# Kernel tuning notes

Measured on AMD Instinct MI355X. Metric: run time of the kernel, lower is better.

The kernel has to match this reference:

```python
import jax, jax.numpy as jnp
import numpy as np
import math

D_MODEL = 2048
N_HEADS = 16
D_K = D_MODEL // N_HEADS


def setup_inputs() -> dict:
    key = jax.random.key(0)
    ks = jax.random.split(key, 10)
    B, S = 1, 2048
    scale = 1.0 / math.sqrt(D_MODEL)
    x = jax.random.normal(ks[0], (B, S, D_MODEL), dtype=jnp.float32)
    mask = jnp.ones((1, 1, S, S), dtype=bool)
    Wq = jax.random.normal(ks[1], (D_MODEL, D_MODEL), dtype=jnp.float32) * scale
    bq = jnp.zeros((D_MODEL,), dtype=jnp.float32)
    Wk = jax.random.normal(ks[2], (D_MODEL, D_MODEL), dtype=jnp.float32) * scale
    bk = jnp.zeros((D_MODEL,), dtype=jnp.float32)
    Wv = jax.random.normal(ks[3], (D_MODEL, D_MODEL), dtype=jnp.float32) * scale
    bv = jnp.zeros((D_MODEL,), dtype=jnp.float32)
    Wo = jax.random.normal(ks[4], (D_MODEL, D_MODEL), dtype=jnp.float32) * scale
    bo = jnp.zeros((D_MODEL,), dtype=jnp.float32)
    return {"x": x, "mask": mask, "Wq": Wq, "bq": bq, "Wk": Wk, "bk": bk,
            "Wv": Wv, "bv": bv, "Wo": Wo, "bo": bo}


def reference(x, mask, Wq, bq, Wk, bk, Wv, bv, Wo, bo):
    B, S, D = x.shape
    # projections (nn.Linear: y = x @ W.T + b; here W stored as [in, out] so x @ W + b)
    def proj(W, b):
        y = x @ W + b                                   # [B, S, D]
        return y.reshape(B, S, N_HEADS, D_K).transpose(0, 2, 1, 3)  # [B, H, S, d_k]
    Q = proj(Wq, bq)
    K = proj(Wk, bk)
    V = proj(Wv, bv)
    scores = jnp.einsum('bhqd,bhkd->bhqk', Q, K) / math.sqrt(D_K)  # [B, H, S, S]
    scores = jnp.where(mask, scores, -jnp.inf)
    attn = jax.nn.softmax(scores, axis=-1)
    out = jnp.einsum('bhqk,bhkd->bhqd', attn, V)        # [B, H, S, d_k]
    out = out.transpose(0, 2, 1, 3).reshape(B, S, D)    # [B, S, D]
    return out @ Wo + bo
```

## Files before the change

kernel.cpp:

```cpp
#include <hip/hip_runtime.h>
#include <cstdint>
#include <cstddef>

typedef __bf16 bf16;
typedef bf16 bf16x8 __attribute__((ext_vector_type(8)));
typedef bf16 bf16x4 __attribute__((ext_vector_type(4)));
typedef bf16 bf16x2 __attribute__((ext_vector_type(2)));
typedef float f32x4 __attribute__((ext_vector_type(4)));
typedef float f32x16 __attribute__((ext_vector_type(16)));
typedef uint32_t u32x4 __attribute__((ext_vector_type(4)));

#define AS1 __attribute__((address_space(1)))
#define AS3 __attribute__((address_space(3)))

constexpr int DMODEL = 2048;
constexpr int SEQ    = 2048;
constexpr int DK     = 128;
constexpr float QSCALE_LOG2E = 0.12751740f;

__global__ __launch_bounds__(256) void cvt_x_kernel(const float* __restrict__ x,
                                                    bf16* __restrict__ xb) {
  size_t i = (size_t)blockIdx.x * 256 + threadIdx.x;
  const float4 a = ((const float4*)x)[i * 2];
  const float4 b = ((const float4*)x)[i * 2 + 1];
  bf16x8 v;
  v[0] = (bf16)a.x; v[1] = (bf16)a.y; v[2] = (bf16)a.z; v[3] = (bf16)a.w;
  v[4] = (bf16)b.x; v[5] = (bf16)b.y; v[6] = (bf16)b.z; v[7] = (bf16)b.w;
  *(bf16x8*)(xb + i * 8) = v;
}

__global__ __launch_bounds__(256) void transpose_w_kernel(
    const float* __restrict__ W0, const float* __restrict__ W1,
    const float* __restrict__ W2, const float* __restrict__ W3,
    bf16* __restrict__ T0, bf16* __restrict__ T1,
    bf16* __restrict__ T2, bf16* __restrict__ T3) {
  int z = blockIdx.x >> 10;
  int t = blockIdx.x & 1023;
  int bi = t >> 5, bj = t & 31;
  const float* W = (z == 0) ? W0 : (z == 1) ? W1 : (z == 2) ? W2 : W3;
  bf16* T        = (z == 0) ? T0 : (z == 1) ? T1 : (z == 2) ? T2 : T3;

  __shared__ float tile[64][68];
  int tid = threadIdx.x;
  int tr = tid >> 4, tc = tid & 15;
#pragma unroll
  for (int i = 0; i < 4; i++) {
    float4 v = *(const float4*)(W + (size_t)(bi * 64 + tr + i * 16) * DMODEL + bj * 64 + tc * 4);
    *(float4*)&tile[tr + i * 16][tc * 4] = v;
  }
  __syncthreads();
  int nl = tid >> 2, kc = (tid & 3) * 16;
  bf16x8 o0, o1;
#pragma unroll
  for (int j = 0; j < 8; j++) {
    o0[j] = (bf16)tile[kc + j][nl];
    o1[j] = (bf16)tile[kc + 8 + j][nl];
  }
  bf16* dst = T + (size_t)(bj * 64 + nl) * DMODEL + bi * 64 + kc;
  *(bf16x8*)dst       = o0;
  *(bf16x8*)(dst + 8) = o1;
}

template <int KIND>
__global__ __launch_bounds__(256) void gemm_bt_kernel(
    const bf16* __restrict__ A,
    const bf16* __restrict__ Bt0, const float* __restrict__ bias0, bf16* __restrict__ outB0,
    const bf16* __restrict__ Bt1, const float* __restrict__ bias1, bf16* __restrict__ outB1,
    const bf16* __restrict__ Bt2, const float* __restrict__ bias2, bf16* __restrict__ outB2,
    float* __restrict__ outF) {
  __shared__ bf16 Als[128 * 64];
  __shared__ bf16 Bls[128 * 64];

  int zt, t;
  if constexpr (KIND == 0) { zt = blockIdx.x >> 8; t = blockIdx.x & 255; }
  else                     { zt = 0;               t = blockIdx.x;       }

  const bf16* Btp; const float* bias;
  if constexpr (KIND == 0) {
    Btp  = (zt == 0) ? Bt0 : (zt == 1) ? Bt1 : Bt2;
    bias = (zt == 0) ? bias0 : (zt == 1) ? bias1 : bias2;
  } else { Btp = Bt0; bias = bias0; }

  int tm = t >> 4, tn = t & 15;
  int m0 = tm * 128, n0 = tn * 128;
  int tid = threadIdx.x;
  int w = tid >> 6, l = tid & 63;
  int wm = w >> 1, wn = w & 1;
  int g = l >> 4, r16 = l & 15;

  f32x4 acc[4][4];
#pragma unroll
  for (int i = 0; i < 4; i++)
#pragma unroll
    for (int j = 0; j < 4; j++) acc[i][j] = (f32x4){0.f, 0.f, 0.f, 0.f};

  int lrow = l >> 3;
  for (int kt = 0; kt < DMODEL / 64; kt++) {
    const bf16* abase = A   + (size_t)m0 * DMODEL + kt * 64;
    const bf16* bbase = Btp + (size_t)n0 * DMODEL + kt * 64;
#pragma unroll
    for (int i = 0; i < 4; i++) {
      int chunk = w * 4 + i;
      int row   = chunk * 8 + lrow;
      int slot  = (l & 7) ^ (row & 7);
      __builtin_amdgcn_global_load_lds((const AS1 void*)(abase + (size_t)row * DMODEL + slot * 8),
                                       (AS3 void*)(Als + chunk * 512), 16, 0, 0);
      __builtin_amdgcn_global_load_lds((const AS1 void*)(bbase + (size_t)row * DMODEL + slot * 8),
                                       (AS3 void*)(Bls + chunk * 512), 16, 0, 0);
    }
    __syncthreads();
#pragma unroll
    for (int ks = 0; ks < 2; ks++) {
      bf16x8 af[4], bfr[4];
#pragma unroll
      for (int mf = 0; mf < 4; mf++) {
        int row  = wm * 64 + mf * 16 + r16;
        int slot = (ks * 4 + g) ^ (row & 7);
        af[mf] = *(const bf16x8*)(Als + row * 64 + slot * 8);
      }
#pragma unroll
      for (int nf = 0; nf < 4; nf++) {
        int row  = wn * 64 + nf * 16 + r16;
        int slot = (ks * 4 + g) ^ (row & 7);
        bfr[nf] = *(const bf16x8*)(Bls + row * 64 + slot * 8);
      }
#pragma unroll
      for (int mf = 0; mf < 4; mf++)
#pragma unroll
        for (int nf = 0; nf < 4; nf++)
          acc[mf][nf] = __builtin_amdgcn_mfma_f32_16x16x32_bf16(af[mf], bfr[nf], acc[mf][nf], 0, 0, 0);
    }
    __syncthreads();
  }

  float bval[4];
#pragma unroll
  for (int nf = 0; nf < 4; nf++) bval[nf] = bias[n0 + wn * 64 + nf * 16 + r16];

  if constexpr (KIND == 1) {
#pragma unroll
    for (int mf = 0; mf < 4; mf++)
#pragma unroll
      for (int nf = 0; nf < 4; nf++)
#pragma unroll
        for (int r = 0; r < 4; r++)
          outF[(size_t)(m0 + wm * 64 + mf * 16 + g * 4 + r) * DMODEL + n0 + wn * 64 + nf * 16 + r16] =
              acc[mf][nf][r] + bval[nf];
  } else {
    if (zt == 2) {
#pragma unroll
      for (int mf = 0; mf < 4; mf++)
#pragma unroll
        for (int nf = 0; nf < 4; nf++) {
          bf16x4 pk;
#pragma unroll
          for (int r = 0; r < 4; r++) pk[r] = (bf16)(acc[mf][nf][r] + bval[nf]);
          *(bf16x4*)(outB2 + (size_t)(n0 + wn * 64 + nf * 16 + r16) * SEQ + m0 + wm * 64 + mf * 16 + g * 4) = pk;
        }
    } else {
      bf16* outp = (zt == 0) ? outB0 : outB1;
      float scl  = (zt == 0) ? QSCALE_LOG2E : 1.0f;
#pragma unroll
      for (int mf = 0; mf < 4; mf++)
#pragma unroll
        for (int nf = 0; nf < 4; nf++)
#pragma unroll
          for (int r = 0; r < 4; r++)
            outp[(size_t)(m0 + wm * 64 + mf * 16 + g * 4 + r) * DMODEL + n0 + wn * 64 + nf * 16 + r16] =
                (bf16)((acc[mf][nf][r] + bval[nf]) * scl);
    }
  }
}

__global__ __launch_bounds__(256, 2) void attn_kernel(const bf16* __restrict__ Q,
                                                      const bf16* __restrict__ K,
                                                      const bf16* __restrict__ Vt,
                                                      float* __restrict__ Opart,
                                                      float* __restrict__ Mp,
                                                      float* __restrict__ Lp) {
  constexpr int NT = 1024 / 64;
  int bx = blockIdx.x;
  int qt = bx >> 5;
  int hh = bx & 31;
  int h = hh >> 1, half = hh & 1;
  int tid = threadIdx.x;
  int w = tid >> 6, l = tid & 63;
  int q5 = l & 31, h5 = l >> 5;

  __shared__ bf16 KL[2][8192];
  __shared__ bf16 VL[2][8192];

  int q0 = qt * 128 + w * 32;

  const bf16* ksrc[4];
  const bf16* vsrc[4];
#pragma unroll
  for (int i = 0; i < 4; i++) {
    int unit = i * 256 + tid;
    ksrc[i] = K  + (size_t)(half * 1024 + (unit & 63)) * DMODEL + h * DK + (unit >> 6) * 8;
    vsrc[i] = Vt + (size_t)(h * DK + (unit & 127)) * SEQ + half * 1024 + (unit >> 7) * 8;
  }

#define ATTN_STAGE(BUF)                                                        \
  {                                                                            \
    _Pragma("unroll")                                                          \
    for (int i_ = 0; i_ < 4; i_++) {                                           \
      __builtin_amdgcn_global_load_lds((const AS1 void*)ksrc[i_],              \
          (AS3 void*)(&KL[BUF][(i_ * 256 + tid) * 8]), 16, 0, 0);              \
      ksrc[i_] += 64 * DMODEL;                                                 \
      __builtin_amdgcn_global_load_lds((const AS1 void*)vsrc[i_],              \
          (AS3 void*)(&VL[BUF][(i_ * 256 + tid) * 8]), 16, 0, 0);              \
      vsrc[i_] += 64;                                                          \
    }                                                                          \
  }

  bf16x8 qb[8];
  {
    const bf16* qbase = Q + (size_t)(q0 + q5) * DMODEL + h * DK + h5 * 8;
#pragma unroll
    for (int kc = 0; kc < 8; kc++) qb[kc] = *(const bf16x8*)(qbase + kc * 16);
  }

  f32x16 o[4];
#pragma unroll
  for (int vf = 0; vf < 4; vf++)
#pragma unroll
    for (int i = 0; i < 16; i++) o[vf][i] = 0.f;
  float mrow = -1e30f, lrow = 0.f;

  ATTN_STAGE(0);
  __syncthreads();

  for (int kb = 0; kb < NT; kb++) {
    int cur = kb & 1;
    if (kb + 1 < NT) ATTN_STAGE(cur ^ 1);

    const bf16* KB = &KL[cur][0];
    f32x16 s0, s1;
#pragma unroll
    for (int i = 0; i < 16; i++) { s0[i] = 0.f; s1[i] = 0.f; }
#pragma unroll
    for (int kc = 0; kc < 8; kc++) {
      bf16x8 k0 = *(const bf16x8*)(KB + ((kc * 2 + h5) * 64 + q5) * 8);
      bf16x8 k1 = *(const bf16x8*)(KB + ((kc * 2 + h5) * 64 + 32 + q5) * 8);
      s0 = __builtin_amdgcn_mfma_f32_32x32x16_bf16(k0, qb[kc], s0, 0, 0, 0);
      s1 = __builtin_amdgcn_mfma_f32_32x32x16_bf16(k1, qb[kc], s1, 0, 0, 0);
    }

    float tm8[8];
#pragma unroll
    for (int i = 0; i < 8; i++)
      tm8[i] = fmaxf(fmaxf(s0[i], s0[i + 8]), fmaxf(s1[i], s1[i + 8]));
#pragma unroll
    for (int i = 0; i < 4; i++) tm8[i] = fmaxf(tm8[i], tm8[i + 4]);
    float bm = fmaxf(fmaxf(tm8[0], tm8[2]), fmaxf(tm8[1], tm8[3]));
    bm = fmaxf(bm, __shfl_xor(bm, 32));

    if (!__all(bm <= mrow + 11.0f)) {
      float mn = fmaxf(mrow, bm);
      float al = exp2f(mrow - mn);
      mrow = mn;
      lrow *= al;
#pragma unroll
      for (int vf = 0; vf < 4; vf++)
#pragma unroll
        for (int i = 0; i < 16; i++) o[vf][i] *= al;
    }

#pragma unroll
    for (int i = 0; i < 16; i++) s0[i] = exp2f(s0[i] - mrow);
#pragma unroll
    for (int i = 0; i < 16; i++) s1[i] = exp2f(s1[i] - mrow);
    float ta[8];
#pragma unroll
    for (int i = 0; i < 8; i++) ta[i] = (s0[i] + s0[i + 8]) + (s1[i] + s1[i + 8]);
#pragma unroll
    for (int i = 0; i < 4; i++) ta[i] += ta[i + 4];
    float ps = (ta[0] + ta[2]) + (ta[1] + ta[3]);
    ps += __shfl_xor(ps, 32);
    lrow += ps;

    uint32_t u[16];
#pragma unroll
    for (int rp = 0; rp < 8; rp++) {
      bf16x2 t0; t0[0] = (bf16)s0[2 * rp]; t0[1] = (bf16)s0[2 * rp + 1];
      u[rp] = __builtin_bit_cast(uint32_t, t0);
      bf16x2 t1; t1[0] = (bf16)s1[2 * rp]; t1[1] = (bf16)s1[2 * rp + 1];
      u[8 + rp] = __builtin_bit_cast(uint32_t, t1);
    }
#pragma unroll
    for (int b = 0; b < 16; b += 4) {
      asm volatile("v_permlane32_swap_b32 %0, %1" : "+v"(u[b]),     "+v"(u[b + 2]));
      asm volatile("v_permlane32_swap_b32 %0, %1" : "+v"(u[b + 1]), "+v"(u[b + 3]));
    }

    const bf16* VB = &VL[cur][0];
#pragma unroll
    for (int ks = 0; ks < 4; ks++) {
      u32x4 tw = {u[ks * 4], u[ks * 4 + 1], u[ks * 4 + 2], u[ks * 4 + 3]};
      bf16x8 pb = __builtin_bit_cast(bf16x8, tw);
#pragma unroll
      for (int vf = 0; vf < 4; vf++) {
        bf16x8 vv = *(const bf16x8*)(VB + ((ks * 2 + h5) * 128 + vf * 32 + q5) * 8);
        o[vf] = __builtin_amdgcn_mfma_f32_32x32x16_bf16(vv, pb, o[vf], 0, 0, 0);
      }
    }
    __syncthreads();
  }

  float* obase = Opart + ((size_t)hh * SEQ + q0 + q5) * DK + h5 * 4;
#pragma unroll
  for (int vf = 0; vf < 4; vf++)
#pragma unroll
    for (int rr = 0; rr < 4; rr++) {
      float4 pk;
      pk.x = o[vf][rr * 4 + 0]; pk.y = o[vf][rr * 4 + 1];
      pk.z = o[vf][rr * 4 + 2]; pk.w = o[vf][rr * 4 + 3];
      *(float4*)(obase + vf * 32 + rr * 8) = pk;
    }
  if (h5 == 0) {
    Mp[(size_t)hh * SEQ + q0 + q5] = mrow;
    Lp[(size_t)hh * SEQ + q0 + q5] = lrow;
  }
#undef ATTN_STAGE
}

__global__ __launch_bounds__(256) void attn_merge_kernel(const float* __restrict__ Opart,
                                                         const float* __restrict__ Mp,
                                                         const float* __restrict__ Lp,
                                                         bf16* __restrict__ AO) {
  size_t idx = (size_t)blockIdx.x * 256 + threadIdx.x;
  int d8 = idx & 15;
  int q  = (int)((idx >> 4) & 2047);
  int h  = (int)(idx >> 15);
  size_t ra = (size_t)(h * 2) * SEQ + q;
  size_t rb = (size_t)(h * 2 + 1) * SEQ + q;
  float ma = Mp[ra], mb = Mp[rb];
  float la = Lp[ra], lb = Lp[rb];
  float m  = fmaxf(ma, mb);
  float wa = exp2f(ma - m), wb = exp2f(mb - m);
  float inv = 1.0f / (la * wa + lb * wb);
  wa *= inv; wb *= inv;
  const float4* A = (const float4*)(Opart + ra * DK + d8 * 8);
  const float4* B = (const float4*)(Opart + rb * DK + d8 * 8);
  float4 a0 = A[0], a1 = A[1], b0 = B[0], b1 = B[1];
  bf16x8 r;
  r[0] = (bf16)(a0.x * wa + b0.x * wb);
  r[1] = (bf16)(a0.y * wa + b0.y * wb);
  r[2] = (bf16)(a0.z * wa + b0.z * wb);
  r[3] = (bf16)(a0.w * wa + b0.w * wb);
  r[4] = (bf16)(a1.x * wa + b1.x * wb);
  r[5] = (bf16)(a1.y * wa + b1.y * wb);
  r[6] = (bf16)(a1.z * wa + b1.z * wb);
  r[7] = (bf16)(a1.w * wa + b1.w * wb);
  *(bf16x8*)(AO + (size_t)q * DMODEL + h * DK + d8 * 8) = r;
}

extern "C" void kernel_launch(void* const* d_in, const int* in_sizes, int n_in,
                              void* d_out, int out_size, void* d_ws, size_t ws_size,
                              hipStream_t stream) {
  const float* x  = (const float*)d_in[0];
  const float* Wq = (const float*)d_in[2];
  const float* bq = (const float*)d_in[3];
  const float* Wk = (const float*)d_in[4];
  const float* bk = (const float*)d_in[5];
  const float* Wv = (const float*)d_in[6];
  const float* bv = (const float*)d_in[7];
  const float* Wo = (const float*)d_in[8];
  const float* bo = (const float*)d_in[9];
  float* out = (float*)d_out;

  const size_t MAT = (size_t)DMODEL * DMODEL;
  bf16* p   = (bf16*)d_ws;
  bf16* xb  = p; p += MAT;
  bf16* Wqt = p; p += MAT;
  bf16* Wkt = p; p += MAT;
  bf16* Wvt = p; p += MAT;
  bf16* Wot = p; p += MAT;
  bf16* Qb  = p; p += MAT;
  bf16* Kb  = p; p += MAT;
  bf16* Vtb = p; p += MAT;
  bf16* AOb = p; p += MAT;
  float* Opart = (float*)xb;
  float* Mpart = (float*)p; p += 512 * 1024 / 2;
  float* Lpart = (float*)p;

  cvt_x_kernel<<<2048, 256, 0, stream>>>(x, xb);
  transpose_w_kernel<<<4096, 256, 0, stream>>>(Wq, Wk, Wv, Wo, Wqt, Wkt, Wvt, Wot);
  gemm_bt_kernel<0><<<768, 256, 0, stream>>>(xb, Wqt, bq, Qb, Wkt, bk, Kb, Wvt, bv, Vtb, nullptr);
  attn_kernel<<<512, 256, 0, stream>>>(Qb, Kb, Vtb, Opart, Mpart, Lpart);
  attn_merge_kernel<<<2048, 256, 0, stream>>>(Opart, Mpart, Lpart, AOb);
  gemm_bt_kernel<1><<<256, 256, 0, stream>>>(AOb, Wot, bo, nullptr,
                                             nullptr, nullptr, nullptr,
                                             nullptr, nullptr, nullptr, out);
}
```

Measured before the change: 207.7 us.

## Replace QKV projection GEMM with 256x256-tile pipelined LDS-direct kernel

Adds a new fused QKV projection kernel that uses 256x256 output tiles with 512 threads. It double-buffers LDS filled by direct global-to-LDS loads with XOR swizzling, interleaves staging with MFMA quadrants, and raises MFMA wave priority with s_setprio. The goal is more operand reuse per tile and better overlap of memory traffic with matrix math. The cost is that only 192 blocks launch, which may underfill the GPU's compute units, and the large LDS and register footprint may limit occupancy.

Result: faster. 197.8 us (-4.8%).

```diff
diff --git a/kernel.cpp b/kernel.cpp
--- a/kernel.cpp
+++ b/kernel.cpp
@@ -59,6 +59,162 @@
   bf16* dst = T + (size_t)(bj * 64 + nl) * DMODEL + bi * 64 + kc;
   *(bf16x8*)dst       = o0;
   *(bf16x8*)(dst + 8) = o1;
+}
+
+__global__ __launch_bounds__(512, 2) void gemm256_qkv_kernel(
+    const bf16* __restrict__ A,
+    const bf16* __restrict__ Bt0, const float* __restrict__ bias0, bf16* __restrict__ outQ,
+    const bf16* __restrict__ Bt1, const float* __restrict__ bias1, bf16* __restrict__ outK,
+    const bf16* __restrict__ Bt2, const float* __restrict__ bias2, bf16* __restrict__ outV) {
+  constexpr int NT = DMODEL / 64;
+  __shared__ bf16 Asl[2][16384];
+  __shared__ bf16 Bsl[2][16384];
+
+  int zt = blockIdx.x >> 6;
+  int t  = blockIdx.x & 63;
+  int tm = t >> 3, tn = t & 7;
+  int m0 = tm * 256, n0 = tn * 256;
+  const bf16* Btp   = (zt == 0) ? Bt0 : (zt == 1) ? Bt1 : Bt2;
+  const float* bias = (zt == 0) ? bias0 : (zt == 1) ? bias1 : bias2;
+
+  int tid = threadIdx.x;
+  int w = tid >> 6, l = tid & 63;
+  int wm = w >> 2, wn = w & 3;
+  int g = l >> 4, r16 = l & 15;
+
+  int u0 = tid, u1 = 512 + tid;
+  int r0 = u0 >> 3, s0 = u0 & 7;
+  int r1 = u1 >> 3, s1 = u1 & 7;
+  const bf16* aS0 = A + (size_t)(m0 + r0) * DMODEL + (s0 ^ (r0 & 7)) * 8;
+  const bf16* aS1 = A + (size_t)(m0 + r1) * DMODEL + (s1 ^ (r1 & 7)) * 8;
+  const bf16* bS0 = Btp + (size_t)(n0 + r0) * DMODEL + (s0 ^ (r0 & 7)) * 8;
+  const bf16* bS1 = Btp + (size_t)(n0 + r1) * DMODEL + (s1 ^ (r1 & 7)) * 8;
+
+  auto STAGE = [&](int tile, int h) {
+    if (tile >= NT) return;
+    int buf = tile & 1;
+    size_t roff = (size_t)(h & 1) * 128 * DMODEL + (size_t)tile * 64;
+    if (h < 2) {
+      __builtin_amdgcn_global_load_lds((const AS1 void*)(aS0 + roff),
+          (AS3 void*)(&Asl[buf][(h & 1) * 8192 + u0 * 8]), 16, 0, 0);
+      __builtin_amdgcn_global_load_lds((const AS1 void*)(aS1 + roff),
+          (AS3 void*)(&Asl[buf][(h & 1) * 8192 + u1 * 8]), 16, 0, 0);
+    } else {
+      __builtin_amdgcn_global_load_lds((const AS1 void*)(bS0 + roff),
+          (AS3 void*)(&Bsl[buf][(h & 1) * 8192 + u0 * 8]), 16, 0, 0);
+      __builtin_amdgcn_global_load_lds((const AS1 void*)(bS1 + roff),
+          (AS3 void*)(&Bsl[buf][(h & 1) * 8192 + u1 * 8]), 16, 0, 0);
+    }
+  };
+
+  bf16x8 afq[2][8];
+  bf16x8 bfn[2][4];
+  f32x4 acc[8][4];
+#pragma unroll
+  for (int i = 0; i < 8; i++)
+#pragma unroll
+    for (int j = 0; j < 4; j++) acc[i][j] = (f32x4){0.f, 0.f, 0.f, 0.f};
+
+#define G256_LDA(MQ, BUF)                                                      \
+  _Pragma("unroll")                                                            \
+  for (int mf = 0; mf < 4; mf++) {                                             \
+    int row = wm * 128 + (MQ) * 64 + mf * 16 + r16;                            \
+    _Pragma("unroll")                                                          \
+    for (int ks = 0; ks < 2; ks++)                                             \
+      afq[MQ][mf * 2 + ks] =                                                   \
+          *(const bf16x8*)(&Asl[BUF][row * 64 + (((ks * 4 + g) ^ (row & 7)) * 8)]); \
+  }
+#define G256_LDB(NQ, BUF)                                                      \
+  _Pragma("unroll")                                                            \
+  for (int nf = 0; nf < 2; nf++) {                                             \
+    int row = wn * 64 + (NQ) * 32 + nf * 16 + r16;                             \
+    _Pragma("unroll")                                                          \
+    for (int ks = 0; ks < 2; ks++)                                             \
+      bfn[NQ][nf * 2 + ks] =                                                   \
+          *(const bf16x8*)(&Bsl[BUF][row * 64 + (((ks * 4 + g) ^ (row & 7)) * 8)]); \
+  }
+#define G256_MMA(MQ, NQ)                                                       \
+  _Pragma("unroll")                                                            \
+  for (int mf = 0; mf < 4; mf++)                                               \
+    _Pragma("unroll")                                                          \
+    for (int nf = 0; nf < 2; nf++)                                             \
+      _Pragma("unroll")                                                        \
+      for (int ks = 0; ks < 2; ks++)                                           \
+        acc[(MQ) * 4 + mf][(NQ) * 2 + nf] =                                    \
+            __builtin_amdgcn_mfma_f32_16x16x32_bf16(afq[MQ][mf * 2 + ks],      \
+                bfn[NQ][nf * 2 + ks], acc[(MQ) * 4 + mf][(NQ) * 2 + nf], 0, 0, 0);
+#define G256_BAR() __builtin_amdgcn_s_barrier()
+#define G256_P1()  __builtin_amdgcn_s_setprio(1)
+#define G256_P0()  __builtin_amdgcn_s_setprio(0)
+
+  STAGE(0, 0); STAGE(0, 1); STAGE(0, 2); STAGE(0, 3);
+  STAGE(1, 0); STAGE(1, 1);
+  asm volatile("s_waitcnt vmcnt(4)" ::: "memory");
+  G256_BAR();
+
+  for (int it = 0; it < NT / 2; ++it) {
+    int t1 = 2 * it + 1, t2 = 2 * it + 2, t3 = 2 * it + 3;
+    G256_LDA(0, 0) G256_LDB(0, 0)
+    STAGE(t1, 2);
+    G256_BAR(); G256_P1(); G256_MMA(0, 0) G256_P0(); G256_BAR();
+    G256_LDA(1, 0) G256_LDB(1, 0)
+    STAGE(t1, 3);
+    G256_BAR(); G256_P1(); G256_MMA(1, 0) G256_P0(); G256_BAR();
+    STAGE(t2, 0);
+    G256_BAR(); G256_P1(); G256_MMA(0, 1) G256_P0(); G256_BAR();
+    STAGE(t2, 1);
+    G256_BAR(); G256_P1(); G256_MMA(1, 1) G256_P0();
+    if (it < NT / 2 - 1) asm volatile("s_waitcnt vmcnt(4)" ::: "memory");
+    else                 asm volatile("s_waitcnt vmcnt(0)" ::: "memory");
+    G256_BAR();
+    G256_LDA(0, 1) G256_LDB(0, 1)
+    STAGE(t2, 2);
+    G256_BAR(); G256_P1(); G256_MMA(0, 0) G256_P0(); G256_BAR();
+    G256_LDA(1, 1) G256_LDB(1, 1)
+    STAGE(t2, 3);
+    G256_BAR(); G256_P1(); G256_MMA(1, 0) G256_P0(); G256_BAR();
+    STAGE(t3, 0);
+    G256_BAR(); G256_P1(); G256_MMA(0, 1) G256_P0(); G256_BAR();
+    STAGE(t3, 1);
+    G256_BAR(); G256_P1(); G256_MMA(1, 1) G256_P0();
+    if (it < NT / 2 - 1) asm volatile("s_waitcnt vmcnt(4)" ::: "memory");
+    G256_BAR();
+  }
+
+  float bval[4];
+#pragma unroll
+  for (int nf = 0; nf < 4; nf++) bval[nf] = bias[n0 + wn * 64 + nf * 16 + r16];
+
+  if (zt == 2) {
+#pragma unroll
+    for (int mf = 0; mf < 8; mf++)
+#pragma unroll
+      for (int nf = 0; nf < 4; nf++) {
+        bf16x4 pk;
+#pragma unroll
+        for (int r = 0; r < 4; r++) pk[r] = (bf16)(acc[mf][nf][r] + bval[nf]);
+        *(bf16x4*)(outV + (size_t)(n0 + wn * 64 + nf * 16 + r16) * SEQ +
+                   m0 + wm * 128 + mf * 16 + g * 4) = pk;
+      }
+  } else {
+    bf16* outp = (zt == 0) ? outQ : outK;
+    float scl  = (zt == 0) ? QSCALE_LOG2E : 1.0f;
+#pragma unroll
+    for (int mf = 0; mf < 8; mf++)
+#pragma unroll
+      for (int nf = 0; nf < 4; nf++)
+#pragma unroll
+        for (int r = 0; r < 4; r++)
+          outp[(size_t)(m0 + wm * 128 + mf * 16 + g * 4 + r) * DMODEL +
+               n0 + wn * 64 + nf * 16 + r16] =
+              (bf16)((acc[mf][nf][r] + bval[nf]) * scl);
+  }
+#undef G256_LDA
+#undef G256_LDB
+#undef G256_MMA
+#undef G256_BAR
+#undef G256_P1
+#undef G256_P0
 }
 
 template <int KIND>
@@ -387,7 +543,7 @@
 
   cvt_x_kernel<<<2048, 256, 0, stream>>>(x, xb);
   transpose_w_kernel<<<4096, 256, 0, stream>>>(Wq, Wk, Wv, Wo, Wqt, Wkt, Wvt, Wot);
-  gemm_bt_kernel<0><<<768, 256, 0, stream>>>(xb, Wqt, bq, Qb, Wkt, bk, Kb, Wvt, bv, Vtb, nullptr);
+  gemm256_qkv_kernel<<<192, 512, 0, stream>>>(xb, Wqt, bq, Qb, Wkt, bk, Kb, Wvt, bv, Vtb);
   attn_kernel<<<512, 256, 0, stream>>>(Qb, Kb, Vtb, Opart, Mpart, Lpart);
   attn_merge_kernel<<<2048, 256, 0, stream>>>(Opart, Mpart, Lpart, AOb);
   gemm_bt_kernel<1><<<256, 256, 0, stream>>>(AOb, Wot, bo, nullptr,
```
